# Optimization experiments

Hardware: AMD Instinct MI355X
Metric: run time of the kernel (lower is better)

The kernel has to match this reference:

```python
import jax, jax.numpy as jnp
import numpy as np

H = 1024
V = 5000
NUM_LAYERS = 2
B, T, U = 2, 128, 64


def setup_inputs() -> dict:
    key = jax.random.key(0)
    ks = jax.random.split(key, 16)
    s = 0.02
    inp = {
        "encoder_out": jax.random.normal(ks[0], (B, T, H), dtype=jnp.float32),
        "targets": jax.random.randint(ks[1], (B, U), 0, V),
        "embed": jax.random.normal(ks[2], (V, H), dtype=jnp.float32) * s,
        # stacked 2-layer LSTM params, PyTorch gate order (i, f, g, o)
        "lstm_Wih": jax.random.normal(ks[3], (NUM_LAYERS, 4 * H, H), dtype=jnp.float32) * s,
        "lstm_Whh": jax.random.normal(ks[4], (NUM_LAYERS, 4 * H, H), dtype=jnp.float32) * s,
        "lstm_bih": jnp.zeros((NUM_LAYERS, 4 * H), dtype=jnp.float32),
        "lstm_bhh": jnp.zeros((NUM_LAYERS, 4 * H), dtype=jnp.float32),
        "enc_W": jax.random.normal(ks[5], (H, H), dtype=jnp.float32) * s,
        "enc_b": jnp.zeros((H,), dtype=jnp.float32),
        "pred_W": jax.random.normal(ks[6], (H, H), dtype=jnp.float32) * s,
        "pred_b": jnp.zeros((H,), dtype=jnp.float32),
        "out_W": jax.random.normal(ks[7], (V + 1, H), dtype=jnp.float32) * s,
        "out_b": jnp.zeros((V + 1,), dtype=jnp.float32),
    }
    return inp


def _lstm_layer(x, Wih, Whh, bih, bhh):
    # x: [B, U, H] -> [B, U, H]; single LSTM layer, PyTorch gate order i,f,g,o
    b, u, h = x.shape
    bias = bih + bhh  # [4H]
    # precompute input projections for all timesteps: [U, B, 4H]
    xg = jnp.einsum('buh,gh->ubg', x, Wih) + bias

    def step(carry, xt):
        hprev, cprev = carry
        gates = xt + hprev @ Whh.T  # [B, 4H]
        i, f, g, o = jnp.split(gates, 4, axis=-1)
        i = jax.nn.sigmoid(i)
        f = jax.nn.sigmoid(f)
        g = jnp.tanh(g)
        o = jax.nn.sigmoid(o)
        c = f * cprev + i * g
        hnew = o * jnp.tanh(c)
        return (hnew, c), hnew

    init = (jnp.zeros((b, h), x.dtype), jnp.zeros((b, h), x.dtype))
    _, hs = jax.lax.scan(step, init, xg)  # hs: [U, B, H]
    return hs.transpose(1, 0, 2)


def reference(encoder_out, targets, embed, lstm_Wih, lstm_Whh, lstm_bih, lstm_bhh,
              enc_W, enc_b, pred_W, pred_b, out_W, out_b):
    # Prediction network: embedding + 2-layer LSTM (deterministic -> no dropout)
    x = embed[targets]  # [B, U, H]
    for l in range(NUM_LAYERS):
        x = _lstm_layer(x, lstm_Wih[l], lstm_Whh[l], lstm_bih[l], lstm_bhh[l])
    pred_out = x  # [B, U, H]

    # Joint network: proj + broadcast add over (T, U) + ReLU + output linear
    enc_p = jnp.einsum('bth,oh->bto', encoder_out, enc_W) + enc_b  # [B, T, H]
    prd_p = jnp.einsum('buh,oh->buo', pred_out, pred_W) + pred_b    # [B, U, H]
    joint = jax.nn.relu(enc_p[:, :, None, :] + prd_p[:, None, :, :])  # [B, T, U, H]
    logits = jnp.einsum('btuh,vh->btuv', joint, out_W) + out_b  # [B, T, U, V+1]
    return logits
```

## Files before the change

kernel.cpp:

```cpp
#include <hip/hip_runtime.h>
#include <hip/hip_bf16.h>

#define B_ 2
#define T_ 128
#define U_ 64
#define H_ 1024
#define NO_ 5001

typedef __attribute__((ext_vector_type(8))) short bf16x8;
typedef __attribute__((ext_vector_type(4))) float f32x4;

__device__ __forceinline__ float bf2f(unsigned short s) {
  unsigned int u = ((unsigned int)s) << 16;
  float f; __builtin_memcpy(&f, &u, 4); return f;
}
__device__ __forceinline__ unsigned short f2bf(float f) {
  unsigned int u; __builtin_memcpy(&u, &f, 4);
  u = u + 0x7FFFu + ((u >> 16) & 1u);
  return (unsigned short)(u >> 16);
}
__device__ __forceinline__ float fsig(float x) {
  x = fminf(fmaxf(x, -30.f), 30.f);
  float e = __expf(-x);
  return __builtin_amdgcn_rcpf(1.f + e);
}
__device__ __forceinline__ float ftanh(float x) {
  x = fminf(fmaxf(x, -15.f), 15.f);
  float e = __expf(2.f * x);
  return (e - 1.f) * __builtin_amdgcn_rcpf(e + 1.f);
}

__device__ __forceinline__ void gload_lds16(const unsigned short* g, unsigned short* l) {
  __builtin_amdgcn_global_load_lds(
      (const __attribute__((address_space(1))) unsigned int*)g,
      (__attribute__((address_space(3))) unsigned int*)l,
      16, 0, 0);
}

#define R_OUTW 1280256
#define R_WIH  (R_OUTW + 2097152)
#define R_WHH  (R_WIH + 2097152)
#define R_ENCW (R_WHH + 262144)
#define R_PRDW (R_ENCW + 262144)
#define R_ENC  (R_PRDW + 65536)
#define R_BIAS (R_ENC + 1280)

__global__ void k_cvt_all(
    const float* __restrict__ outW, const float* __restrict__ Wih,
    const float* __restrict__ Whh,  const float* __restrict__ encW,
    const float* __restrict__ prdW, const float* __restrict__ enc,
    const float* __restrict__ outB,
    unsigned short* __restrict__ outW_bf, unsigned short* __restrict__ Wih_bf,
    unsigned short* __restrict__ Whh_bf,  unsigned short* __restrict__ encW_bf,
    unsigned short* __restrict__ prdW_bf, unsigned short* __restrict__ enc_bf,
    float* __restrict__ biasPad)
{
  int i = blockIdx.x * 256 + threadIdx.x;
  const float* src; unsigned short* dst; int off;
  if (i < R_OUTW)      { src = outW; dst = outW_bf; off = i; }
  else if (i < R_WIH)  { src = Wih;  dst = Wih_bf;  off = i - R_OUTW; }
  else if (i < R_WHH)  { src = Whh;  dst = Whh_bf;  off = i - R_WIH; }
  else if (i < R_ENCW) { src = encW; dst = encW_bf; off = i - R_WHH; }
  else if (i < R_PRDW) { src = prdW; dst = prdW_bf; off = i - R_ENCW; }
  else if (i < R_ENC)  { src = enc;  dst = enc_bf;  off = i - R_PRDW; }
  else {
    int e0 = (i - R_ENC) * 4;
    float4 v;
    v.x = (e0 + 0 < NO_) ? outB[e0 + 0] : 0.f;
    v.y = (e0 + 1 < NO_) ? outB[e0 + 1] : 0.f;
    v.z = (e0 + 2 < NO_) ? outB[e0 + 2] : 0.f;
    v.w = (e0 + 3 < NO_) ? outB[e0 + 3] : 0.f;
    *(float4*)&biasPad[e0] = v;
    return;
  }
  const float4 v = ((const float4*)src)[off];
  ushort4 o;
  o.x = f2bf(v.x); o.y = f2bf(v.y); o.z = f2bf(v.z); o.w = f2bf(v.w);
  ((ushort4*)dst)[off] = o;
}

__global__ void k_embed(const int* __restrict__ tg, const float* __restrict__ em,
                        unsigned short* __restrict__ x0) {
  int idx = blockIdx.x * 256 + threadIdx.x;
  int bu = idx >> 8;
  int kc = (idx & 255) << 2;
  int t = tg[bu];
  const float4 v = *(const float4*)&em[(long)t * H_ + kc];
  ushort4 o; o.x = f2bf(v.x); o.y = f2bf(v.y); o.z = f2bf(v.z); o.w = f2bf(v.w);
  *(ushort4*)&x0[bu * H_ + kc] = o;
}

__global__ __launch_bounds__(256) void gemm_proj(
    const unsigned short* __restrict__ enc_bf, const unsigned short* __restrict__ x2_bf,
    const unsigned short* __restrict__ encW_bf, const unsigned short* __restrict__ prdW_bf,
    const float* __restrict__ encB, const float* __restrict__ prdB,
    float* __restrict__ ep, float* __restrict__ pp)
{
  __shared__ unsigned short As[128 * 32];
  __shared__ unsigned short Bs[128 * 32];
  const int tid = threadIdx.x;
  const unsigned short* A; const unsigned short* W; const float* b1; float* C;
  int m0;
  if (blockIdx.y < 2) { A = enc_bf; W = encW_bf; b1 = encB; C = ep; m0 = blockIdx.y * 128; }
  else                { A = x2_bf;  W = prdW_bf; b1 = prdB; C = pp; m0 = 0; }
  const int n0 = blockIdx.x * 128;
  const int K = H_, N = H_;
  const int lane = tid & 63, w = tid >> 6;
  const int wr = (w >> 1) * 64, wc = (w & 1) * 64;
  const int lr = lane & 15, lk = (lane >> 4) * 8;
  f32x4 acc[4][4] = {};

  for (int k0 = 0; k0 < K; k0 += 32) {
#pragma unroll
    for (int s = 0; s < 2; ++s) {
      int idx = (w * 2 + s) * 64 + lane;
      int row = idx >> 2, c8 = (idx & 3) * 8;
      gload_lds16(&A[(long)(m0 + row) * K + k0 + c8], &As[(w * 2 + s) * 512]);
      gload_lds16(&W[(long)(n0 + row) * K + k0 + c8], &Bs[(w * 2 + s) * 512]);
    }
    __syncthreads();
    bf16x8 aF[4], bF[4];
#pragma unroll
    for (int i = 0; i < 4; ++i) {
      aF[i] = *(const bf16x8*)&As[(wr + i * 16 + lr) * 32 + lk];
      bF[i] = *(const bf16x8*)&Bs[(wc + i * 16 + lr) * 32 + lk];
    }
#pragma unroll
    for (int i = 0; i < 4; ++i)
#pragma unroll
      for (int j = 0; j < 4; ++j)
        acc[i][j] = __builtin_amdgcn_mfma_f32_16x16x32_bf16(aF[i], bF[j], acc[i][j], 0, 0, 0);
    __syncthreads();
  }

  const int lq = (lane >> 4) * 4;
#pragma unroll
  for (int j = 0; j < 4; ++j) {
    int col = n0 + wc + j * 16 + lr;
    float bb = b1[col];
#pragma unroll
    for (int i = 0; i < 4; ++i) {
      int rowg = m0 + wr + i * 16 + lq;
#pragma unroll
      for (int r = 0; r < 4; ++r)
        C[(long)(rowg + r) * N + col] = acc[i][j][r] + bb;
    }
  }
}

#define STAGE_A(kt2, kh, rb) \
  gload_lds16(aSrc[rb] + (kt2) * 64 + (kh) * 32, \
              &As_f[((((kt2) & 1) * 2 + (kh)) * 8192) + ((rb) * 128 + wv * 16) * 32])
#define STAGE_B(kt2, kh, rb) \
  gload_lds16(bSrc[rb] + (kt2) * 64 + (kh) * 32, \
              &Bs_f[((((kt2) & 1) * 2 + (kh)) * 8192) + ((rb) * 128 + wv * 16) * 32])

__global__ __launch_bounds__(512, 1) void gemm_logits(
    const unsigned short* __restrict__ A, const unsigned short* __restrict__ W,
    const float* __restrict__ biasPad, float* __restrict__ C, int M, int N, int K)
{
  __shared__ __align__(16) unsigned short lds_all[65536];
  unsigned short* As_f = lds_all;
  unsigned short* Bs_f = lds_all + 32768;
  const int tid = threadIdx.x;
  const int lane = tid & 63, wv = tid >> 6;
  const int wm = wv >> 2, wn = wv & 3;
  int swzb = (blockIdx.x & 7) * 160 + (blockIdx.x >> 3);
  const int n0 = (swzb >> 6) * 256;
  const int m0 = (swzb & 63) * 256;
  const int NT = K / 64;

  const unsigned short* aSrc[2];
  const unsigned short* bSrc[2];
#pragma unroll
  for (int rb = 0; rb < 2; ++rb) {
    int rl = rb * 128 + (tid >> 2);
    int c2s = (tid & 3) ^ ((rl >> 1) & 3);
    aSrc[rb] = A + (long)(m0 + rl) * K + c2s * 8;
    bSrc[rb] = W + (long)(n0 + rl) * K + c2s * 8;
  }
  int aOff[8], bOff[4];
#pragma unroll
  for (int i = 0; i < 8; ++i) {
    int r = wm * 128 + i * 16 + (lane & 15);
    aOff[i] = r * 32 + (((lane >> 4) ^ ((r >> 1) & 3)) * 8);
  }
#pragma unroll
  for (int j = 0; j < 4; ++j) {
    int r = wn * 64 + j * 16 + (lane & 15);
    bOff[j] = r * 32 + (((lane >> 4) ^ ((r >> 1) & 3)) * 8);
  }

  f32x4 acc[8][4] = {};

  STAGE_A(0, 0, 0); STAGE_A(0, 0, 1); STAGE_B(0, 0, 0); STAGE_B(0, 0, 1);
  STAGE_A(0, 1, 0); STAGE_A(0, 1, 1); STAGE_B(0, 1, 0); STAGE_B(0, 1, 1);

  for (int kt = 0; kt < NT; ++kt) {
    const int b = kt & 1;
    asm volatile("s_waitcnt vmcnt(4)" ::: "memory");
    __builtin_amdgcn_s_barrier();
    __builtin_amdgcn_sched_barrier(0);
    {
      const int base = (b * 2 + 0) * 8192;
      bf16x8 aF[8], bF[4];
#pragma unroll
      for (int i = 0; i < 8; ++i) aF[i] = *(const bf16x8*)&As_f[base + aOff[i]];
#pragma unroll
      for (int j = 0; j < 4; ++j) bF[j] = *(const bf16x8*)&Bs_f[base + bOff[j]];
      if (kt + 1 < NT) {
        STAGE_A(kt + 1, 0, 0); STAGE_A(kt + 1, 0, 1);
        STAGE_B(kt + 1, 0, 0); STAGE_B(kt + 1, 0, 1);
        STAGE_A(kt + 1, 1, 0); STAGE_A(kt + 1, 1, 1);
      }
      __builtin_amdgcn_s_setprio(1);
#pragma unroll
      for (int i = 0; i < 8; ++i)
#pragma unroll
        for (int j = 0; j < 4; ++j)
          acc[i][j] = __builtin_amdgcn_mfma_f32_16x16x32_bf16(aF[i], bF[j], acc[i][j], 0, 0, 0);
      __builtin_amdgcn_s_setprio(0);
    }
    if (kt + 1 < NT) { asm volatile("s_waitcnt vmcnt(6)" ::: "memory"); }
    else             { asm volatile("s_waitcnt vmcnt(0)" ::: "memory"); }
    __builtin_amdgcn_s_barrier();
    __builtin_amdgcn_sched_barrier(0);
    {
      const int base = (b * 2 + 1) * 8192;
      bf16x8 aF[8], bF[4];
#pragma unroll
      for (int i = 0; i < 8; ++i) aF[i] = *(const bf16x8*)&As_f[base + aOff[i]];
#pragma unroll
      for (int j = 0; j < 4; ++j) bF[j] = *(const bf16x8*)&Bs_f[base + bOff[j]];
      if (kt + 1 < NT) { STAGE_B(kt + 1, 1, 0); STAGE_B(kt + 1, 1, 1); }
      __builtin_amdgcn_s_setprio(1);
#pragma unroll
      for (int i = 0; i < 8; ++i)
#pragma unroll
        for (int j = 0; j < 4; ++j)
          acc[i][j] = __builtin_amdgcn_mfma_f32_16x16x32_bf16(aF[i], bF[j], acc[i][j], 0, 0, 0);
      __builtin_amdgcn_s_setprio(0);
    }
  }

  float* eb = (float*)lds_all;
  const int lq = (lane >> 4) * 4;
  float bv4[4];
#pragma unroll
  for (int j = 0; j < 4; ++j) bv4[j] = biasPad[n0 + wn * 64 + j * 16 + (lane & 15)];

#pragma unroll
  for (int cp = 0; cp < 4; ++cp) {
    __syncthreads();
#pragma unroll
    for (int ii = 0; ii < 2; ++ii) {
      int rbase = wm * 32 + ii * 16 + lq;
#pragma unroll
      for (int j = 0; j < 4; ++j) {
        int col = wn * 64 + j * 16 + (lane & 15);
#pragma unroll
        for (int r = 0; r < 4; ++r)
          eb[(rbase + r) * 261 + col] = acc[cp * 2 + ii][j][r] + bv4[j];
      }
    }
    __syncthreads();
    {
      int rl = tid >> 3, ci = tid & 7;
      long grow = (long)m0 + (rl >> 5) * 128 + cp * 32 + (rl & 31);
      float* crow = C + grow * N + n0;
      const float* er = &eb[rl * 261];
#pragma unroll
      for (int k = 0; k < 8; ++k) {
        int col = ci * 4 + k * 32;
        float4 v = *(const float4*)&er[col];
        int gc = n0 + col;
        if (gc + 4 <= N) {
          *(float4*)&crow[col] = v;
        } else if (gc < N) {
          float tmp[4] = {v.x, v.y, v.z, v.w};
#pragma unroll
          for (int e = 0; e < 4; ++e)
            if (gc + e < N) crow[col + e] = tmp[e];
        }
      }
    }
  }
}

__global__ __launch_bounds__(256, 1) void lstm_fused3(
    const unsigned short* __restrict__ x0_bf,
    const unsigned short* __restrict__ Whh0,
    const unsigned short* __restrict__ Wih0,
    const unsigned short* __restrict__ Whh1,
    const unsigned short* __restrict__ Wih1,
    const float* __restrict__ bih0, const float* __restrict__ bhh0,
    const float* __restrict__ bih1, const float* __restrict__ bhh1,
    unsigned short* __restrict__ x2_bf,
    float* __restrict__ hbuf0,
    float* __restrict__ hbuf1,
    float* __restrict__ xbuf,
    float* __restrict__ xg1buf, int* __restrict__ flags1,
    float* __restrict__ xg0buf, int* __restrict__ flags0)
{
  __shared__ float hs[2][H_];
  __shared__ float part[2][4][64][2];
  __shared__ float biasS[64];

  const int tid = threadIdx.x;
  const int grp = blockIdx.x >> 6;
  const int bid = blockIdx.x & 63;
  const int w = tid >> 6, l = tid & 63;
  const int g = l >> 4, q = l & 15;
  const int row = g * 1024 + bid * 16 + q;
  const int kb = w * 256;

#define DOT_BODY(WREG, SRC)                                                              \
  _Pragma("unroll")                                                                      \
  for (int it = 0; it < 32; ++it) {                                                      \
    bf16x8 wv = WREG[it];                                                                \
    float4 h0a = *(const float4*)&SRC[0][kb + it * 8];                                   \
    float4 h0b = *(const float4*)&SRC[0][kb + it * 8 + 4];                               \
    float4 h1a = *(const float4*)&SRC[1][kb + it * 8];                                   \
    float4 h1b = *(const float4*)&SRC[1][kb + it * 8 + 4];                               \
    a00 += bf2f((unsigned short)wv[0]) * h0a.x + bf2f((unsigned short)wv[4]) * h0b.x;    \
    a01 += bf2f((unsigned short)wv[1]) * h0a.y + bf2f((unsigned short)wv[5]) * h0b.y;    \
    a02 += bf2f((unsigned short)wv[2]) * h0a.z + bf2f((unsigned short)wv[6]) * h0b.z;    \
    a03 += bf2f((unsigned short)wv[3]) * h0a.w + bf2f((unsigned short)wv[7]) * h0b.w;    \
    a10 += bf2f((unsigned short)wv[0]) * h1a.x + bf2f((unsigned short)wv[4]) * h1b.x;    \
    a11 += bf2f((unsigned short)wv[1]) * h1a.y + bf2f((unsigned short)wv[5]) * h1b.y;    \
    a12 += bf2f((unsigned short)wv[2]) * h1a.z + bf2f((unsigned short)wv[6]) * h1b.z;    \
    a13 += bf2f((unsigned short)wv[3]) * h1a.w + bf2f((unsigned short)wv[7]) * h1b.w;    \
  }

  if (grp == 0 || grp == 2) {
    const unsigned short* Whh = (grp == 0) ? Whh0 : Whh1;
    float* hbuf   = (grp == 0) ? hbuf0 : hbuf1;
    const float* xgbufR = (grp == 0) ? xg0buf : xg1buf;
    const int* flagsR   = (grp == 0) ? flags0 : flags1;
    bf16x8 wreg[32];
#pragma unroll
    for (int it = 0; it < 32; ++it)
      wreg[it] = *(const bf16x8*)&Whh[(long)row * H_ + kb + it * 8];
    __syncthreads();

    float creg = 0.f;
    for (int u = 0; u < U_; ++u) {
      const int p = u & 1;
      float xgi = 0.f, xgf = 0.f, xgg = 0.f, xgo = 0.f;
      if (tid < 32) {
        const int* fp = &flagsR[(u * 64 + bid) * 16];
        int fv;
        for (;;) {
          asm volatile("global_load_dword %0, %1, off sc1\n\ts_waitcnt vmcnt(0)"
                       : "=v"(fv) : "v"(fp) : "memory");
          if (fv != 0) break;
          __builtin_amdgcn_s_sleep(8);
        }
        const float* xb = &xgbufR[((u * 64 + bid) * 2 + (tid >> 4)) * 64];
        int qq = tid & 15;
        asm volatile("global_load_dword %0, %1, off sc1" : "=&v"(xgi) : "v"(xb + qq) : "memory");
        asm volatile("global_load_dword %0, %1, off sc1" : "=&v"(xgf) : "v"(xb + 16 + qq) : "memory");
        asm volatile("global_load_dword %0, %1, off sc1" : "=&v"(xgg) : "v"(xb + 32 + qq) : "memory");
        asm volatile("global_load_dword %0, %1, off sc1" : "=&v"(xgo) : "v"(xb + 48 + qq) : "memory");
      }
      float a00 = 0.f, a01 = 0.f, a02 = 0.f, a03 = 0.f;
      float a10 = 0.f, a11 = 0.f, a12 = 0.f, a13 = 0.f;
      if (u > 0) {
        const float thr = 4.0f * u - 2.0f;
        const float* base = hbuf + (u & 1) * 2 * H_;
        const float* pa = base + tid * 4;
        const float* pb = base + H_ + tid * 4;
        float4 va, vb;
        for (;;) {
          asm volatile("global_load_dwordx4 %0, %2, off sc1\n\t"
                       "global_load_dwordx4 %1, %3, off sc1\n\t"
                       "s_waitcnt vmcnt(0)"
                       : "=v"(va), "=v"(vb) : "v"(pa), "v"(pb) : "memory");
          if (va.x > thr && va.y > thr && va.z > thr && va.w > thr &&
              vb.x > thr && vb.y > thr && vb.z > thr && vb.w > thr) break;
          __builtin_amdgcn_s_sleep(8);
        }
        const float off = 4.0f * u;
        va.x -= off; va.y -= off; va.z -= off; va.w -= off;
        vb.x -= off; vb.y -= off; vb.z -= off; vb.w -= off;
        *(float4*)&hs[0][tid * 4] = va;
        *(float4*)&hs[1][tid * 4] = vb;
        DOT_BODY(wreg, hs)
      }
      part[p][w][l][0] = (a00 + a01) + (a02 + a03);
      part[p][w][l][1] = (a10 + a11) + (a12 + a13);
      if (tid < 32) {
        asm volatile("s_waitcnt vmcnt(0)"
                     : "+v"(xgi), "+v"(xgf), "+v"(xgg), "+v"(xgo) :: "memory");
      }
      __syncthreads();
      if (tid < 32) {
        int b = tid >> 4, qq = tid & 15;
        float gi = part[p][0][qq][b] + part[p][1][qq][b] + part[p][2][qq][b]
                 + part[p][3][qq][b] + xgi;
        float gf = part[p][0][16 + qq][b] + part[p][1][16 + qq][b] + part[p][2][16 + qq][b]
                 + part[p][3][16 + qq][b] + xgf;
        float gc = part[p][0][32 + qq][b] + part[p][1][32 + qq][b] + part[p][2][32 + qq][b]
                 + part[p][3][32 + qq][b] + xgg;
        float go = part[p][0][48 + qq][b] + part[p][1][48 + qq][b] + part[p][2][48 + qq][b]
                 + part[p][3][48 + qq][b] + xgo;
        float i_ = fsig(gi), f_ = fsig(gf), g_ = ftanh(gc), o_ = fsig(go);
        creg = f_ * creg + i_ * g_;
        float h = o_ * ftanh(creg);
        int j = bid * 16 + qq;
        if (grp == 0) {
          float tvx = h + 4.0f;
          const float* px = &xbuf[u * 2 * H_ + b * H_ + j];
          asm volatile("global_store_dword %0, %1, off sc1" :: "v"(px), "v"(tvx) : "memory");
        } else {
          x2_bf[(b * U_ + u) * H_ + j] = f2bf(h);
        }
        if (u < U_ - 1) {
          float tv = h + 4.0f * (u + 1);
          const float* pp2 = &hbuf[((u + 1) & 1) * 2 * H_ + b * H_ + j];
          asm volatile("global_store_dword %0, %1, off sc1" :: "v"(pp2), "v"(tv) : "memory");
        }
      }
    }
  } else {
    const bool isX1 = (grp == 1);
    const unsigned short* Wih = isX1 ? Wih1 : Wih0;
    const float* bihp = isX1 ? bih1 : bih0;
    const float* bhhp = isX1 ? bhh1 : bhh0;
    float* xgbufW = isX1 ? xg1buf : xg0buf;
    int* flagsW   = isX1 ? flags1 : flags0;
    bf16x8 wreg[32];
#pragma unroll
    for (int it = 0; it < 32; ++it)
      wreg[it] = *(const bf16x8*)&Wih[(long)row * H_ + kb + it * 8];
    if (tid < 64) {
      int rr = (tid >> 4) * 1024 + bid * 16 + (tid & 15);
      biasS[tid] = bihp[rr] + bhhp[rr];
    }
    __syncthreads();

    for (int u = 0; u < U_; ++u) {
      const int p = u & 1;
      if (isX1) {
        const float* base = xbuf + u * 2 * H_;
        const float* pa = base + tid * 4;
        const float* pb = base + H_ + tid * 4;
        float4 va, vb;
        for (;;) {
          asm volatile("global_load_dwordx4 %0, %2, off sc1\n\t"
                       "global_load_dwordx4 %1, %3, off sc1\n\t"
                       "s_waitcnt vmcnt(0)"
                       : "=v"(va), "=v"(vb) : "v"(pa), "v"(pb) : "memory");
          if (va.x > 2.f && va.y > 2.f && va.z > 2.f && va.w > 2.f &&
              vb.x > 2.f && vb.y > 2.f && vb.z > 2.f && vb.w > 2.f) break;
          __builtin_amdgcn_s_sleep(8);
        }
        va.x -= 4.f; va.y -= 4.f; va.z -= 4.f; va.w -= 4.f;
        vb.x -= 4.f; vb.y -= 4.f; vb.z -= 4.f; vb.w -= 4.f;
        *(float4*)&hs[0][tid * 4] = va;
        *(float4*)&hs[1][tid * 4] = vb;
      } else {
        ushort4 xa = *(const ushort4*)&x0_bf[(0 * U_ + u) * H_ + tid * 4];
        ushort4 xb = *(const ushort4*)&x0_bf[(1 * U_ + u) * H_ + tid * 4];
        float4 va, vb;
        va.x = bf2f(xa.x); va.y = bf2f(xa.y); va.z = bf2f(xa.z); va.w = bf2f(xa.w);
        vb.x = bf2f(xb.x); vb.y = bf2f(xb.y); vb.z = bf2f(xb.z); vb.w = bf2f(xb.w);
        *(float4*)&hs[0][tid * 4] = va;
        *(float4*)&hs[1][tid * 4] = vb;
      }

      float a00 = 0.f, a01 = 0.f, a02 = 0.f, a03 = 0.f;
      float a10 = 0.f, a11 = 0.f, a12 = 0.f, a13 = 0.f;
      DOT_BODY(wreg, hs)
      part[p][w][l][0] = (a00 + a01) + (a02 + a03);
      part[p][w][l][1] = (a10 + a11) + (a12 + a13);
      __syncthreads();
      if (tid < 128) {
        int b = tid >> 6, ll = tid & 63;
        float s = part[p][0][ll][b] + part[p][1][ll][b] + part[p][2][ll][b]
                + part[p][3][ll][b] + biasS[ll];
        const float* pw = &xgbufW[((u * 64 + bid) * 2 + b) * 64 + ll];
        asm volatile("global_store_dword %0, %1, off sc1" :: "v"(pw), "v"(s) : "memory");
        asm volatile("s_waitcnt vmcnt(0)" ::: "memory");
      }
      __syncthreads();
      if (tid == 0) {
        int one = 1;
        const int* fp = &flagsW[(u * 64 + bid) * 16];
        asm volatile("global_store_dword %0, %1, off sc1" :: "v"(fp), "v"(one) : "memory");
      }
    }
  }
#undef DOT_BODY
}

__global__ void k_joint(const float* __restrict__ ep, const float* __restrict__ pp,
                        unsigned short* __restrict__ jt)
{
  int idx = blockIdx.x * 256 + threadIdx.x;
  int m = idx >> 8;
  int kc = (idx & 255) << 2;
  int erow = m >> 6;
  int prow = (m >> 13) * U_ + (m & 63);
  const float4 e = *(const float4*)&ep[erow * H_ + kc];
  const float4 p = *(const float4*)&pp[prow * H_ + kc];
  float4 s;
  s.x = fmaxf(e.x + p.x, 0.f); s.y = fmaxf(e.y + p.y, 0.f);
  s.z = fmaxf(e.z + p.z, 0.f); s.w = fmaxf(e.w + p.w, 0.f);
  ushort4 o; o.x = f2bf(s.x); o.y = f2bf(s.y); o.z = f2bf(s.z); o.w = f2bf(s.w);
  *(ushort4*)&jt[m * H_ + kc] = o;
}

extern "C" void kernel_launch(void* const* d_in, const int* in_sizes, int n_in,
                              void* d_out, int out_size, void* d_ws, size_t ws_size,
                              hipStream_t stream)
{
  const float* enc   = (const float*)d_in[0];
  const int*   tg    = (const int*)d_in[1];
  const float* em    = (const float*)d_in[2];
  const float* Wih   = (const float*)d_in[3];
  const float* Whh   = (const float*)d_in[4];
  const float* bih   = (const float*)d_in[5];
  const float* bhh   = (const float*)d_in[6];
  const float* encW  = (const float*)d_in[7];
  const float* encB  = (const float*)d_in[8];
  const float* prdW  = (const float*)d_in[9];
  const float* prdB  = (const float*)d_in[10];
  const float* outW  = (const float*)d_in[11];
  const float* outB  = (const float*)d_in[12];
  float* out = (float*)d_out;
  char* ws = (char*)d_ws;

  unsigned short* outW_bf = (unsigned short*)(ws + 0);
  unsigned short* Wih_bf  = (unsigned short*)(ws + 10485760);
  unsigned short* Whh_bf  = (unsigned short*)(ws + 27262976);
  unsigned short* encW_bf = (unsigned short*)(ws + 44040192);
  unsigned short* prdW_bf = (unsigned short*)(ws + 46137344);
  unsigned short* enc_bf  = (unsigned short*)(ws + 48234496);
  unsigned short* x0_bf   = (unsigned short*)(ws + 48758784);
  unsigned short* x2_bf   = (unsigned short*)(ws + 49283072);
  float* xg1buf = (float*)(ws + 49545216);
  float* hbufL0 = (float*)(ws + 51642368);
  unsigned short* jt = (unsigned short*)(ws + 51659008);
  int*   flags0 = (int*)(ws + 51659008);
  float* xg0buf = (float*)(ws + 51659008 + 262144);
  float* hbufL1 = (float*)(ws + 85213440);
  float* biasPad = (float*)(ws + 85229824);
  float* xbuf = (float*)(ws + 85250304);
  int* flags1 = (int*)(ws + 85774592);
  float* ep = (float*)(ws + 49545216);
  float* pp = (float*)(ws + 49545216 + 1048576);

  hipMemsetAsync(hbufL0, 0, 16384, stream);
  hipMemsetAsync(hbufL1, 0, 86036736 - 85213440, stream);
  hipMemsetAsync(flags0, 0, 262144, stream);

  k_cvt_all<<<R_BIAS / 256, 256, 0, stream>>>(
      outW, Wih, Whh, encW, prdW, enc, outB,
      outW_bf, Wih_bf, Whh_bf, encW_bf, prdW_bf, enc_bf, biasPad);
  k_embed<<<(B_ * U_ * H_ / 4) / 256, 256, 0, stream>>>(tg, em, x0_bf);

  lstm_fused3<<<256, 256, 0, stream>>>(
      x0_bf,
      Whh_bf, Wih_bf,
      Whh_bf + 4096 * H_, Wih_bf + 4096 * H_,
      bih, bhh, bih + 4096, bhh + 4096,
      x2_bf, hbufL0, hbufL1, xbuf,
      xg1buf, flags1, xg0buf, flags0);

  gemm_proj<<<dim3(8, 3), 256, 0, stream>>>(enc_bf, x2_bf, encW_bf, prdW_bf,
                                            encB, prdB, ep, pp);

  k_joint<<<16384, 256, 0, stream>>>(ep, pp, jt);
  gemm_logits<<<1280, 512, 0, stream>>>(jt, outW_bf, biasPad, out, B_ * T_ * U_, NO_, H_);
}
```

Before: 599.5 us.

## Fuse pred projection and joint logits GEMM into persistent LSTM megakernel

Merges the LSTM, the prediction projection and the logits GEMM into one persistent kernel. Extra blocks consume per-timestep LSTM outputs through flag and tag polling, so the projection and the output GEMM overlap with the sequential recurrence. The joint add+ReLU is done on the fly while staging the A tile, which removes the materialised joint buffer. The cost is replacing the tuned 256x256 double-buffered logits GEMM with a simple 128x128 single-buffer loop. Correctness and progress also depend on all 592 blocks being co-resident so the spin-waits cannot deadlock.

```diff
diff --git a/kernel.cpp b/kernel.cpp
--- a/kernel.cpp
+++ b/kernel.cpp
@@ -90,20 +90,14 @@
   *(ushort4*)&x0[bu * H_ + kc] = o;
 }
 
-__global__ __launch_bounds__(256) void gemm_proj(
-    const unsigned short* __restrict__ enc_bf, const unsigned short* __restrict__ x2_bf,
-    const unsigned short* __restrict__ encW_bf, const unsigned short* __restrict__ prdW_bf,
-    const float* __restrict__ encB, const float* __restrict__ prdB,
-    float* __restrict__ ep, float* __restrict__ pp)
+__global__ __launch_bounds__(256) void gemm_ep(
+    const unsigned short* __restrict__ enc_bf, const unsigned short* __restrict__ encW_bf,
+    const float* __restrict__ encB, float* __restrict__ ep)
 {
   __shared__ unsigned short As[128 * 32];
   __shared__ unsigned short Bs[128 * 32];
   const int tid = threadIdx.x;
-  const unsigned short* A; const unsigned short* W; const float* b1; float* C;
-  int m0;
-  if (blockIdx.y < 2) { A = enc_bf; W = encW_bf; b1 = encB; C = ep; m0 = blockIdx.y * 128; }
-  else                { A = x2_bf;  W = prdW_bf; b1 = prdB; C = pp; m0 = 0; }
-  const int n0 = blockIdx.x * 128;
+  const int n0 = blockIdx.x * 128, m0 = blockIdx.y * 128;
   const int K = H_, N = H_;
   const int lane = tid & 63, w = tid >> 6;
   const int wr = (w >> 1) * 64, wc = (w & 1) * 64;
@@ -115,8 +109,8 @@
     for (int s = 0; s < 2; ++s) {
       int idx = (w * 2 + s) * 64 + lane;
       int row = idx >> 2, c8 = (idx & 3) * 8;
-      gload_lds16(&A[(long)(m0 + row) * K + k0 + c8], &As[(w * 2 + s) * 512]);
-      gload_lds16(&W[(long)(n0 + row) * K + k0 + c8], &Bs[(w * 2 + s) * 512]);
+      gload_lds16(&enc_bf[(long)(m0 + row) * K + k0 + c8], &As[(w * 2 + s) * 512]);
+      gload_lds16(&encW_bf[(long)(n0 + row) * K + k0 + c8], &Bs[(w * 2 + s) * 512]);
     }
     __syncthreads();
     bf16x8 aF[4], bF[4];
@@ -137,177 +131,40 @@
 #pragma unroll
   for (int j = 0; j < 4; ++j) {
     int col = n0 + wc + j * 16 + lr;
-    float bb = b1[col];
+    float bb = encB[col];
 #pragma unroll
     for (int i = 0; i < 4; ++i) {
       int rowg = m0 + wr + i * 16 + lq;
 #pragma unroll
       for (int r = 0; r < 4; ++r)
-        C[(long)(rowg + r) * N + col] = acc[i][j][r] + bb;
+        ep[(long)(rowg + r) * N + col] = acc[i][j][r] + bb;
     }
   }
 }
 
-#define STAGE_A(kt2, kh, rb) \
-  gload_lds16(aSrc[rb] + (kt2) * 64 + (kh) * 32, \
-              &As_f[((((kt2) & 1) * 2 + (kh)) * 8192) + ((rb) * 128 + wv * 16) * 32])
-#define STAGE_B(kt2, kh, rb) \
-  gload_lds16(bSrc[rb] + (kt2) * 64 + (kh) * 32, \
-              &Bs_f[((((kt2) & 1) * 2 + (kh)) * 8192) + ((rb) * 128 + wv * 16) * 32])
-
-__global__ __launch_bounds__(512, 1) void gemm_logits(
-    const unsigned short* __restrict__ A, const unsigned short* __restrict__ W,
-    const float* __restrict__ biasPad, float* __restrict__ C, int M, int N, int K)
-{
-  __shared__ __align__(16) unsigned short lds_all[65536];
-  unsigned short* As_f = lds_all;
-  unsigned short* Bs_f = lds_all + 32768;
-  const int tid = threadIdx.x;
-  const int lane = tid & 63, wv = tid >> 6;
-  const int wm = wv >> 2, wn = wv & 3;
-  int swzb = (blockIdx.x & 7) * 160 + (blockIdx.x >> 3);
-  const int n0 = (swzb >> 6) * 256;
-  const int m0 = (swzb & 63) * 256;
-  const int NT = K / 64;
-
-  const unsigned short* aSrc[2];
-  const unsigned short* bSrc[2];
-#pragma unroll
-  for (int rb = 0; rb < 2; ++rb) {
-    int rl = rb * 128 + (tid >> 2);
-    int c2s = (tid & 3) ^ ((rl >> 1) & 3);
-    aSrc[rb] = A + (long)(m0 + rl) * K + c2s * 8;
-    bSrc[rb] = W + (long)(n0 + rl) * K + c2s * 8;
-  }
-  int aOff[8], bOff[4];
-#pragma unroll
-  for (int i = 0; i < 8; ++i) {
-    int r = wm * 128 + i * 16 + (lane & 15);
-    aOff[i] = r * 32 + (((lane >> 4) ^ ((r >> 1) & 3)) * 8);
-  }
-#pragma unroll
-  for (int j = 0; j < 4; ++j) {
-    int r = wn * 64 + j * 16 + (lane & 15);
-    bOff[j] = r * 32 + (((lane >> 4) ^ ((r >> 1) & 3)) * 8);
-  }
-
-  f32x4 acc[8][4] = {};
-
-  STAGE_A(0, 0, 0); STAGE_A(0, 0, 1); STAGE_B(0, 0, 0); STAGE_B(0, 0, 1);
-  STAGE_A(0, 1, 0); STAGE_A(0, 1, 1); STAGE_B(0, 1, 0); STAGE_B(0, 1, 1);
-
-  for (int kt = 0; kt < NT; ++kt) {
-    const int b = kt & 1;
-    asm volatile("s_waitcnt vmcnt(4)" ::: "memory");
-    __builtin_amdgcn_s_barrier();
-    __builtin_amdgcn_sched_barrier(0);
-    {
-      const int base = (b * 2 + 0) * 8192;
-      bf16x8 aF[8], bF[4];
-#pragma unroll
-      for (int i = 0; i < 8; ++i) aF[i] = *(const bf16x8*)&As_f[base + aOff[i]];
-#pragma unroll
-      for (int j = 0; j < 4; ++j) bF[j] = *(const bf16x8*)&Bs_f[base + bOff[j]];
-      if (kt + 1 < NT) {
-        STAGE_A(kt + 1, 0, 0); STAGE_A(kt + 1, 0, 1);
-        STAGE_B(kt + 1, 0, 0); STAGE_B(kt + 1, 0, 1);
-        STAGE_A(kt + 1, 1, 0); STAGE_A(kt + 1, 1, 1);
-      }
-      __builtin_amdgcn_s_setprio(1);
-#pragma unroll
-      for (int i = 0; i < 8; ++i)
-#pragma unroll
-        for (int j = 0; j < 4; ++j)
-          acc[i][j] = __builtin_amdgcn_mfma_f32_16x16x32_bf16(aF[i], bF[j], acc[i][j], 0, 0, 0);
-      __builtin_amdgcn_s_setprio(0);
-    }
-    if (kt + 1 < NT) { asm volatile("s_waitcnt vmcnt(6)" ::: "memory"); }
-    else             { asm volatile("s_waitcnt vmcnt(0)" ::: "memory"); }
-    __builtin_amdgcn_s_barrier();
-    __builtin_amdgcn_sched_barrier(0);
-    {
-      const int base = (b * 2 + 1) * 8192;
-      bf16x8 aF[8], bF[4];
-#pragma unroll
-      for (int i = 0; i < 8; ++i) aF[i] = *(const bf16x8*)&As_f[base + aOff[i]];
-#pragma unroll
-      for (int j = 0; j < 4; ++j) bF[j] = *(const bf16x8*)&Bs_f[base + bOff[j]];
-      if (kt + 1 < NT) { STAGE_B(kt + 1, 1, 0); STAGE_B(kt + 1, 1, 1); }
-      __builtin_amdgcn_s_setprio(1);
-#pragma unroll
-      for (int i = 0; i < 8; ++i)
-#pragma unroll
-        for (int j = 0; j < 4; ++j)
-          acc[i][j] = __builtin_amdgcn_mfma_f32_16x16x32_bf16(aF[i], bF[j], acc[i][j], 0, 0, 0);
-      __builtin_amdgcn_s_setprio(0);
-    }
-  }
-
-  float* eb = (float*)lds_all;
-  const int lq = (lane >> 4) * 4;
-  float bv4[4];
-#pragma unroll
-  for (int j = 0; j < 4; ++j) bv4[j] = biasPad[n0 + wn * 64 + j * 16 + (lane & 15)];
-
-#pragma unroll
-  for (int cp = 0; cp < 4; ++cp) {
-    __syncthreads();
-#pragma unroll
-    for (int ii = 0; ii < 2; ++ii) {
-      int rbase = wm * 32 + ii * 16 + lq;
-#pragma unroll
-      for (int j = 0; j < 4; ++j) {
-        int col = wn * 64 + j * 16 + (lane & 15);
-#pragma unroll
-        for (int r = 0; r < 4; ++r)
-          eb[(rbase + r) * 261 + col] = acc[cp * 2 + ii][j][r] + bv4[j];
-      }
-    }
-    __syncthreads();
-    {
-      int rl = tid >> 3, ci = tid & 7;
-      long grow = (long)m0 + (rl >> 5) * 128 + cp * 32 + (rl & 31);
-      float* crow = C + grow * N + n0;
-      const float* er = &eb[rl * 261];
-#pragma unroll
-      for (int k = 0; k < 8; ++k) {
-        int col = ci * 4 + k * 32;
-        float4 v = *(const float4*)&er[col];
-        int gc = n0 + col;
-        if (gc + 4 <= N) {
-          *(float4*)&crow[col] = v;
-        } else if (gc < N) {
-          float tmp[4] = {v.x, v.y, v.z, v.w};
-#pragma unroll
-          for (int e = 0; e < 4; ++e)
-            if (gc + e < N) crow[col + e] = tmp[e];
-        }
-      }
-    }
-  }
-}
-
-__global__ __launch_bounds__(256, 1) void lstm_fused3(
+__global__ __launch_bounds__(256, 1) void mega(
     const unsigned short* __restrict__ x0_bf,
-    const unsigned short* __restrict__ Whh0,
-    const unsigned short* __restrict__ Wih0,
-    const unsigned short* __restrict__ Whh1,
-    const unsigned short* __restrict__ Wih1,
+    const unsigned short* __restrict__ Whh0, const unsigned short* __restrict__ Wih0,
+    const unsigned short* __restrict__ Whh1, const unsigned short* __restrict__ Wih1,
+    const unsigned short* __restrict__ prdW_bf, const unsigned short* __restrict__ outW_bf,
     const float* __restrict__ bih0, const float* __restrict__ bhh0,
     const float* __restrict__ bih1, const float* __restrict__ bhh1,
-    unsigned short* __restrict__ x2_bf,
-    float* __restrict__ hbuf0,
-    float* __restrict__ hbuf1,
+    const float* __restrict__ prdB, const float* __restrict__ biasPad,
+    const float* __restrict__ ep,
+    float* __restrict__ hbuf0, float* __restrict__ hbuf1,
     float* __restrict__ xbuf,
     float* __restrict__ xg1buf, int* __restrict__ flags1,
-    float* __restrict__ xg0buf, int* __restrict__ flags0)
+    float* __restrict__ xg0buf, int* __restrict__ flags0,
+    float* __restrict__ x2tag,
+    float* __restrict__ ppbuf, int* __restrict__ flagsP,
+    float* __restrict__ out)
 {
-  __shared__ float hs[2][H_];
-  __shared__ float part[2][4][64][2];
-  __shared__ float biasS[64];
+  __shared__ __align__(16) char smem[20992];
+  float (*hs)[H_] = (float(*)[H_])smem;
+  float (*part)[4][64][2] = (float(*)[4][64][2])(smem + 8192);
+  float* biasS = (float*)(smem + 8192 + 4096);
 
   const int tid = threadIdx.x;
-  const int grp = blockIdx.x >> 6;
   const int bid = blockIdx.x & 63;
   const int w = tid >> 6, l = tid & 63;
   const int g = l >> 4, q = l & 15;
@@ -332,7 +189,8 @@
     a13 += bf2f((unsigned short)wv[3]) * h1a.w + bf2f((unsigned short)wv[7]) * h1b.w;    \
   }
 
-  if (grp == 0 || grp == 2) {
+  if (blockIdx.x < 256 && ((blockIdx.x >> 6) == 0 || (blockIdx.x >> 6) == 2)) {
+    const int grp = blockIdx.x >> 6;
     const unsigned short* Whh = (grp == 0) ? Whh0 : Whh1;
     float* hbuf   = (grp == 0) ? hbuf0 : hbuf1;
     const float* xgbufR = (grp == 0) ? xg0buf : xg1buf;
@@ -408,12 +266,13 @@
         creg = f_ * creg + i_ * g_;
         float h = o_ * ftanh(creg);
         int j = bid * 16 + qq;
+        float tvx = h + 4.0f;
         if (grp == 0) {
-          float tvx = h + 4.0f;
           const float* px = &xbuf[u * 2 * H_ + b * H_ + j];
           asm volatile("global_store_dword %0, %1, off sc1" :: "v"(px), "v"(tvx) : "memory");
         } else {
-          x2_bf[(b * U_ + u) * H_ + j] = f2bf(h);
+          const float* px = &x2tag[u * 2 * H_ + b * H_ + j];
+          asm volatile("global_store_dword %0, %1, off sc1" :: "v"(px), "v"(tvx) : "memory");
         }
         if (u < U_ - 1) {
           float tv = h + 4.0f * (u + 1);
@@ -422,8 +281,8 @@
         }
       }
     }
-  } else {
-    const bool isX1 = (grp == 1);
+  } else if (blockIdx.x < 256) {
+    const bool isX1 = ((blockIdx.x >> 6) == 1);
     const unsigned short* Wih = isX1 ? Wih1 : Wih0;
     const float* bihp = isX1 ? bih1 : bih0;
     const float* bhhp = isX1 ? bhh1 : bhh0;
@@ -490,25 +349,179 @@
         asm volatile("global_store_dword %0, %1, off sc1" :: "v"(fp), "v"(one) : "memory");
       }
     }
+  } else if (blockIdx.x < 272) {
+    const int pbid = blockIdx.x - 256;
+    bf16x8 wreg[32];
+#pragma unroll
+    for (int it = 0; it < 32; ++it)
+      wreg[it] = *(const bf16x8*)&prdW_bf[(long)(pbid * 64 + l) * H_ + kb + it * 8];
+    if (tid < 64) biasS[tid] = prdB[pbid * 64 + tid];
+    __syncthreads();
+
+    for (int u = 0; u < U_; ++u) {
+      const int p = u & 1;
+      const float* base = x2tag + u * 2 * H_;
+      const float* pa = base + tid * 4;
+      const float* pb = base + H_ + tid * 4;
+      float4 va, vb;
+      for (;;) {
+        asm volatile("global_load_dwordx4 %0, %2, off sc1\n\t"
+                     "global_load_dwordx4 %1, %3, off sc1\n\t"
+                     "s_waitcnt vmcnt(0)"
+                     : "=v"(va), "=v"(vb) : "v"(pa), "v"(pb) : "memory");
+        if (va.x > 2.f && va.y > 2.f && va.z > 2.f && va.w > 2.f &&
+            vb.x > 2.f && vb.y > 2.f && vb.z > 2.f && vb.w > 2.f) break;
+        __builtin_amdgcn_s_sleep(8);
+      }
+      va.x -= 4.f; va.y -= 4.f; va.z -= 4.f; va.w -= 4.f;
+      vb.x -= 4.f; vb.y -= 4.f; vb.z -= 4.f; vb.w -= 4.f;
+      *(float4*)&hs[0][tid * 4] = va;
+      *(float4*)&hs[1][tid * 4] = vb;
+
+      float a00 = 0.f, a01 = 0.f, a02 = 0.f, a03 = 0.f;
+      float a10 = 0.f, a11 = 0.f, a12 = 0.f, a13 = 0.f;
+      DOT_BODY(wreg, hs)
+      part[p][w][l][0] = (a00 + a01) + (a02 + a03);
+      part[p][w][l][1] = (a10 + a11) + (a12 + a13);
+      __syncthreads();
+      if (tid < 128) {
+        int b = tid >> 6, ll = tid & 63;
+        float s = part[p][0][ll][b] + part[p][1][ll][b] + part[p][2][ll][b]
+                + part[p][3][ll][b] + biasS[ll];
+        const float* pw = &ppbuf[((u * 16 + pbid) * 2 + b) * 64 + ll];
+        asm volatile("global_store_dword %0, %1, off sc1" :: "v"(pw), "v"(s) : "memory");
+        asm volatile("s_waitcnt vmcnt(0)" ::: "memory");
+      }
+      __syncthreads();
+      if (tid == 0) {
+        int one = 1;
+        const int* fp = &flagsP[(u * 16 + pbid) * 16];
+        asm volatile("global_store_dword %0, %1, off sc1" :: "v"(fp), "v"(one) : "memory");
+      }
+    }
+  } else {
+    const int lgid = blockIdx.x - 272;
+    const int col80 = lgid % 80;
+    const int uc = lgid / 80;
+    const int bb = col80 & 1;
+    const int np = col80 >> 1;
+    const int n0 = np * 128;
+    unsigned short* As = (unsigned short*)smem;
+    unsigned short* Bs = (unsigned short*)(smem + 8192);
+    float* eb  = (float*)smem;
+    float* pps = (float*)(smem + 16896);
+    const int lane = tid & 63, w4 = tid >> 6;
+    const int wr = (w4 >> 1) * 64, wc = (w4 & 1) * 64;
+    const int lr = lane & 15, lk = (lane >> 4) * 8;
+    const int lq = (lane >> 4) * 4;
+    float bv[4];
+#pragma unroll
+    for (int j = 0; j < 4; ++j) bv[j] = biasPad[n0 + wc + j * 16 + lr];
+
+    for (int u = uc * 16; u < uc * 16 + 16; ++u) {
+      {
+        int fv = 1;
+        const int* fp = &flagsP[(u * 16 + (lane & 15)) * 16];
+        for (;;) {
+          if (lane < 16) {
+            asm volatile("global_load_dword %0, %1, off sc1\n\ts_waitcnt vmcnt(0)"
+                         : "=v"(fv) : "v"(fp) : "memory");
+          }
+          if (__all(fv != 0)) break;
+          __builtin_amdgcn_s_sleep(8);
+        }
+      }
+      __syncthreads();
+      {
+        int col = tid * 4, pbid = col >> 6, off = col & 63;
+        const float* pa2 = &ppbuf[((u * 16 + pbid) * 2 + bb) * 64 + off];
+        float4 pv;
+        asm volatile("global_load_dwordx4 %0, %1, off sc1\n\ts_waitcnt vmcnt(0)"
+                     : "=v"(pv) : "v"(pa2) : "memory");
+        *(float4*)&pps[col] = pv;
+      }
+      __syncthreads();
+
+      f32x4 acc[4][4] = {};
+      for (int kt = 0; kt < 32; ++kt) {
+        const int k0 = kt * 32;
+#pragma unroll
+        for (int rep = 0; rep < 4; ++rep) {
+          int idx = rep * 256 + tid;
+          int arow = idx >> 3, c4 = (idx & 7) * 4;
+          float4 ev = *(const float4*)&ep[(long)(bb * 128 + arow) * H_ + k0 + c4];
+          float4 pv = *(const float4*)&pps[k0 + c4];
+          ushort4 o;
+          o.x = f2bf(fmaxf(ev.x + pv.x, 0.f));
+          o.y = f2bf(fmaxf(ev.y + pv.y, 0.f));
+          o.z = f2bf(fmaxf(ev.z + pv.z, 0.f));
+          o.w = f2bf(fmaxf(ev.w + pv.w, 0.f));
+          *(ushort4*)&As[arow * 32 + c4] = o;
+        }
+#pragma unroll
+        for (int s2 = 0; s2 < 2; ++s2) {
+          int idx = (w4 * 2 + s2) * 64 + lane;
+          int brow = idx >> 2, c8 = (idx & 3) * 8;
+          gload_lds16(&outW_bf[(long)(n0 + brow) * H_ + k0 + c8], &Bs[(w4 * 2 + s2) * 512]);
+        }
+        __syncthreads();
+        bf16x8 aF[4], bF[4];
+#pragma unroll
+        for (int i = 0; i < 4; ++i) {
+          aF[i] = *(const bf16x8*)&As[(wr + i * 16 + lr) * 32 + lk];
+          bF[i] = *(const bf16x8*)&Bs[(wc + i * 16 + lr) * 32 + lk];
+        }
+#pragma unroll
+        for (int i = 0; i < 4; ++i)
+#pragma unroll
+          for (int j = 0; j < 4; ++j)
+            acc[i][j] = __builtin_amdgcn_mfma_f32_16x16x32_bf16(aF[i], bF[j], acc[i][j], 0, 0, 0);
+        __syncthreads();
+      }
+#pragma unroll
+      for (int cp = 0; cp < 4; ++cp) {
+        __syncthreads();
+        if ((wr == 0) == (cp < 2)) {
+#pragma unroll
+          for (int ii = 0; ii < 2; ++ii) {
+            int i = (cp & 1) * 2 + ii;
+#pragma unroll
+            for (int j = 0; j < 4; ++j) {
+              int col = wc + j * 16 + lr;
+#pragma unroll
+              for (int r = 0; r < 4; ++r) {
+                int lrow = wr + i * 16 + lq + r - cp * 32;
+                eb[lrow * 132 + col] = acc[i][j][r] + bv[j];
+              }
+            }
+          }
+        }
+        __syncthreads();
+        {
+          int rt = tid >> 3, ci = tid & 7;
+          int trow = cp * 32 + rt;
+          long grow = ((long)(bb * 128 + trow)) * 64 + u;
+          float* crow = out + grow * NO_ + n0;
+          const float* er = &eb[rt * 132];
+#pragma unroll
+          for (int k2 = 0; k2 < 4; ++k2) {
+            int col = ci * 4 + k2 * 32;
+            float4 v = *(const float4*)&er[col];
+            int gc = n0 + col;
+            if (gc + 4 <= NO_) {
+              *(float4*)&crow[col] = v;
+            } else if (gc < NO_) {
+              float tmp[4] = {v.x, v.y, v.z, v.w};
+#pragma unroll
+              for (int e = 0; e < 4; ++e)
+                if (gc + e < NO_) crow[col + e] = tmp[e];
+            }
+          }
+        }
+      }
+    }
   }
 #undef DOT_BODY
-}
-
-__global__ void k_joint(const float* __restrict__ ep, const float* __restrict__ pp,
-                        unsigned short* __restrict__ jt)
-{
-  int idx = blockIdx.x * 256 + threadIdx.x;
-  int m = idx >> 8;
-  int kc = (idx & 255) << 2;
-  int erow = m >> 6;
-  int prow = (m >> 13) * U_ + (m & 63);
-  const float4 e = *(const float4*)&ep[erow * H_ + kc];
-  const float4 p = *(const float4*)&pp[prow * H_ + kc];
-  float4 s;
-  s.x = fmaxf(e.x + p.x, 0.f); s.y = fmaxf(e.y + p.y, 0.f);
-  s.z = fmaxf(e.z + p.z, 0.f); s.w = fmaxf(e.w + p.w, 0.f);
-  ushort4 o; o.x = f2bf(s.x); o.y = f2bf(s.y); o.z = f2bf(s.z); o.w = f2bf(s.w);
-  *(ushort4*)&jt[m * H_ + kc] = o;
 }
 
 extern "C" void kernel_launch(void* const* d_in, const int* in_sizes, int n_in,
@@ -538,39 +551,39 @@
   unsigned short* prdW_bf = (unsigned short*)(ws + 46137344);
   unsigned short* enc_bf  = (unsigned short*)(ws + 48234496);
   unsigned short* x0_bf   = (unsigned short*)(ws + 48758784);
-  unsigned short* x2_bf   = (unsigned short*)(ws + 49283072);
   float* xg1buf = (float*)(ws + 49545216);
   float* hbufL0 = (float*)(ws + 51642368);
-  unsigned short* jt = (unsigned short*)(ws + 51659008);
   int*   flags0 = (int*)(ws + 51659008);
-  float* xg0buf = (float*)(ws + 51659008 + 262144);
+  float* xg0buf = (float*)(ws + 51921152);
+  float* x2tag  = (float*)(ws + 54018304);
+  float* ppbuf  = (float*)(ws + 54542592);
+  int*   flagsP = (int*)(ws + 55066880);
+  float* ep     = (float*)(ws + 55132416);
   float* hbufL1 = (float*)(ws + 85213440);
   float* biasPad = (float*)(ws + 85229824);
   float* xbuf = (float*)(ws + 85250304);
   int* flags1 = (int*)(ws + 85774592);
-  float* ep = (float*)(ws + 49545216);
-  float* pp = (float*)(ws + 49545216 + 1048576);
 
   hipMemsetAsync(hbufL0, 0, 16384, stream);
   hipMemsetAsync(hbufL1, 0, 86036736 - 85213440, stream);
   hipMemsetAsync(flags0, 0, 262144, stream);
+  hipMemsetAsync(x2tag, 0, 524288, stream);
+  hipMemsetAsync(flagsP, 0, 65536, stream);
 
   k_cvt_all<<<R_BIAS / 256, 256, 0, stream>>>(
       outW, Wih, Whh, encW, prdW, enc, outB,
       outW_bf, Wih_bf, Whh_bf, encW_bf, prdW_bf, enc_bf, biasPad);
   k_embed<<<(B_ * U_ * H_ / 4) / 256, 256, 0, stream>>>(tg, em, x0_bf);
-
-  lstm_fused3<<<256, 256, 0, stream>>>(
+  gemm_ep<<<dim3(8, 2), 256, 0, stream>>>(enc_bf, encW_bf, encB, ep);
+
+  mega<<<592, 256, 0, stream>>>(
       x0_bf,
       Whh_bf, Wih_bf,
       Whh_bf + 4096 * H_, Wih_bf + 4096 * H_,
+      prdW_bf, outW_bf,
       bih, bhh, bih + 4096, bhh + 4096,
-      x2_bf, hbufL0, hbufL1, xbuf,
-      xg1buf, flags1, xg0buf, flags0);
-
-  gemm_proj<<<dim3(8, 3), 256, 0, stream>>>(enc_bf, x2_bf, encW_bf, prdW_bf,
-                                            encB, prdB, ep, pp);
-
-  k_joint<<<16384, 256, 0, stream>>>(ep, pp, jt);
-  gemm_logits<<<1280, 512, 0, stream>>>(jt, outW_bf, biasPad, out, B_ * T_ * U_, NO_, H_);
-}
+      prdB, biasPad, ep,
+      hbufL0, hbufL1, xbuf,
+      xg1buf, flags1, xg0buf, flags0,
+      x2tag, ppbuf, flagsP, out);
+}
```

Measured after the change: 1.519 ms. 2.53x slower.

## Fuse joint add+ReLU into logits GEMM A-tile build; merge embed into convert kernel

Applied to the files above, without the earlier changes.

The separate joint kernel, which wrote a 16384x1024 bf16 tensor, is removed. The logits GEMM now builds its A tiles directly from the fp32 encoder and prediction projections, doing the add, ReLU and bf16 conversion while storing into LDS. This avoids writing and re-reading a 32MB intermediate, at the cost of synchronous register loads and ALU work inside the pipelined GEMM loop in place of async global-to-LDS loads. The embedding gather is also folded into the conversion kernel to save one launch.

```diff
diff --git a/kernel.cpp b/kernel.cpp
--- a/kernel.cpp
+++ b/kernel.cpp
@@ -44,16 +44,18 @@
 #define R_PRDW (R_ENCW + 262144)
 #define R_ENC  (R_PRDW + 65536)
 #define R_BIAS (R_ENC + 1280)
+#define R_EMB  (R_BIAS + 32768)
 
 __global__ void k_cvt_all(
     const float* __restrict__ outW, const float* __restrict__ Wih,
     const float* __restrict__ Whh,  const float* __restrict__ encW,
     const float* __restrict__ prdW, const float* __restrict__ enc,
     const float* __restrict__ outB,
+    const int* __restrict__ tg, const float* __restrict__ em,
     unsigned short* __restrict__ outW_bf, unsigned short* __restrict__ Wih_bf,
     unsigned short* __restrict__ Whh_bf,  unsigned short* __restrict__ encW_bf,
     unsigned short* __restrict__ prdW_bf, unsigned short* __restrict__ enc_bf,
-    float* __restrict__ biasPad)
+    float* __restrict__ biasPad, unsigned short* __restrict__ x0_bf)
 {
   int i = blockIdx.x * 256 + threadIdx.x;
   const float* src; unsigned short* dst; int off;
@@ -63,7 +65,7 @@
   else if (i < R_ENCW) { src = encW; dst = encW_bf; off = i - R_WHH; }
   else if (i < R_PRDW) { src = prdW; dst = prdW_bf; off = i - R_ENCW; }
   else if (i < R_ENC)  { src = enc;  dst = enc_bf;  off = i - R_PRDW; }
-  else {
+  else if (i < R_BIAS) {
     int e0 = (i - R_ENC) * 4;
     float4 v;
     v.x = (e0 + 0 < NO_) ? outB[e0 + 0] : 0.f;
@@ -72,22 +74,20 @@
     v.w = (e0 + 3 < NO_) ? outB[e0 + 3] : 0.f;
     *(float4*)&biasPad[e0] = v;
     return;
+  } else {
+    int idx = i - R_BIAS;
+    int bu = idx >> 8;
+    int kc = (idx & 255) << 2;
+    int t = tg[bu];
+    const float4 v = *(const float4*)&em[(long)t * H_ + kc];
+    ushort4 o; o.x = f2bf(v.x); o.y = f2bf(v.y); o.z = f2bf(v.z); o.w = f2bf(v.w);
+    *(ushort4*)&x0_bf[bu * H_ + kc] = o;
+    return;
   }
   const float4 v = ((const float4*)src)[off];
   ushort4 o;
   o.x = f2bf(v.x); o.y = f2bf(v.y); o.z = f2bf(v.z); o.w = f2bf(v.w);
   ((ushort4*)dst)[off] = o;
-}
-
-__global__ void k_embed(const int* __restrict__ tg, const float* __restrict__ em,
-                        unsigned short* __restrict__ x0) {
-  int idx = blockIdx.x * 256 + threadIdx.x;
-  int bu = idx >> 8;
-  int kc = (idx & 255) << 2;
-  int t = tg[bu];
-  const float4 v = *(const float4*)&em[(long)t * H_ + kc];
-  ushort4 o; o.x = f2bf(v.x); o.y = f2bf(v.y); o.z = f2bf(v.z); o.w = f2bf(v.w);
-  *(ushort4*)&x0[bu * H_ + kc] = o;
 }
 
 __global__ __launch_bounds__(256) void gemm_proj(
@@ -148,16 +148,14 @@
   }
 }
 
-#define STAGE_A(kt2, kh, rb) \
-  gload_lds16(aSrc[rb] + (kt2) * 64 + (kh) * 32, \
-              &As_f[((((kt2) & 1) * 2 + (kh)) * 8192) + ((rb) * 128 + wv * 16) * 32])
 #define STAGE_B(kt2, kh, rb) \
   gload_lds16(bSrc[rb] + (kt2) * 64 + (kh) * 32, \
               &Bs_f[((((kt2) & 1) * 2 + (kh)) * 8192) + ((rb) * 128 + wv * 16) * 32])
 
-__global__ __launch_bounds__(512, 1) void gemm_logits(
-    const unsigned short* __restrict__ A, const unsigned short* __restrict__ W,
-    const float* __restrict__ biasPad, float* __restrict__ C, int M, int N, int K)
+__global__ __launch_bounds__(512, 1) void gemm_logits_f(
+    const float* __restrict__ ep, const float* __restrict__ pp,
+    const unsigned short* __restrict__ W,
+    const float* __restrict__ biasPad, float* __restrict__ C)
 {
   __shared__ __align__(16) unsigned short lds_all[65536];
   unsigned short* As_f = lds_all;
@@ -168,16 +166,15 @@
   int swzb = (blockIdx.x & 7) * 160 + (blockIdx.x >> 3);
   const int n0 = (swzb >> 6) * 256;
   const int m0 = (swzb & 63) * 256;
-  const int NT = K / 64;
-
-  const unsigned short* aSrc[2];
+  const int NT = H_ / 64;
+  const int N = NO_;
+
   const unsigned short* bSrc[2];
 #pragma unroll
   for (int rb = 0; rb < 2; ++rb) {
     int rl = rb * 128 + (tid >> 2);
     int c2s = (tid & 3) ^ ((rl >> 1) & 3);
-    aSrc[rb] = A + (long)(m0 + rl) * K + c2s * 8;
-    bSrc[rb] = W + (long)(n0 + rl) * K + c2s * 8;
+    bSrc[rb] = W + (long)(n0 + rl) * H_ + c2s * 8;
   }
   int aOff[8], bOff[4];
 #pragma unroll
@@ -191,14 +188,47 @@
     bOff[j] = r * 32 + (((lane >> 4) ^ ((r >> 1) & 3)) * 8);
   }
 
+  const int rA = tid >> 1;
+  const int halfa = tid & 1;
+  const float* eprow = ep + (long)((m0 >> 6) + (rA >> 6)) * H_;
+  const float* pprow = pp + (long)(((m0 >> 13) << 6) + (rA & 63)) * H_;
+  const int abase = rA * 32;
+  const int axor = (rA >> 1) & 3;
+
+  auto BUILD_A = [&](int kt2, int kh) {
+    const int k0 = kt2 * 64 + kh * 32;
+    const int bufb = ((kt2 & 1) * 2 + kh) * 8192;
+#pragma unroll
+    for (int s = 0; s < 2; ++s) {
+      int cc = halfa * 2 + s;
+      int c8 = k0 + cc * 8;
+      float4 e0 = *(const float4*)&eprow[c8];
+      float4 e1 = *(const float4*)&eprow[c8 + 4];
+      float4 p0 = *(const float4*)&pprow[c8];
+      float4 p1 = *(const float4*)&pprow[c8 + 4];
+      ushort4 o0, o1;
+      o0.x = f2bf(fmaxf(e0.x + p0.x, 0.f));
+      o0.y = f2bf(fmaxf(e0.y + p0.y, 0.f));
+      o0.z = f2bf(fmaxf(e0.z + p0.z, 0.f));
+      o0.w = f2bf(fmaxf(e0.w + p0.w, 0.f));
+      o1.x = f2bf(fmaxf(e1.x + p1.x, 0.f));
+      o1.y = f2bf(fmaxf(e1.y + p1.y, 0.f));
+      o1.z = f2bf(fmaxf(e1.z + p1.z, 0.f));
+      o1.w = f2bf(fmaxf(e1.w + p1.w, 0.f));
+      int slot = cc ^ axor;
+      *(ushort4*)&As_f[bufb + abase + slot * 8] = o0;
+      *(ushort4*)&As_f[bufb + abase + slot * 8 + 4] = o1;
+    }
+  };
+
   f32x4 acc[8][4] = {};
 
-  STAGE_A(0, 0, 0); STAGE_A(0, 0, 1); STAGE_B(0, 0, 0); STAGE_B(0, 0, 1);
-  STAGE_A(0, 1, 0); STAGE_A(0, 1, 1); STAGE_B(0, 1, 0); STAGE_B(0, 1, 1);
+  BUILD_A(0, 0); BUILD_A(0, 1);
+  STAGE_B(0, 0, 0); STAGE_B(0, 0, 1); STAGE_B(0, 1, 0); STAGE_B(0, 1, 1);
 
   for (int kt = 0; kt < NT; ++kt) {
     const int b = kt & 1;
-    asm volatile("s_waitcnt vmcnt(4)" ::: "memory");
+    asm volatile("s_waitcnt vmcnt(2)" ::: "memory");
     __builtin_amdgcn_s_barrier();
     __builtin_amdgcn_sched_barrier(0);
     {
@@ -209,9 +239,8 @@
 #pragma unroll
       for (int j = 0; j < 4; ++j) bF[j] = *(const bf16x8*)&Bs_f[base + bOff[j]];
       if (kt + 1 < NT) {
-        STAGE_A(kt + 1, 0, 0); STAGE_A(kt + 1, 0, 1);
+        BUILD_A(kt + 1, 0);
         STAGE_B(kt + 1, 0, 0); STAGE_B(kt + 1, 0, 1);
-        STAGE_A(kt + 1, 1, 0); STAGE_A(kt + 1, 1, 1);
       }
       __builtin_amdgcn_s_setprio(1);
 #pragma unroll
@@ -221,7 +250,7 @@
           acc[i][j] = __builtin_amdgcn_mfma_f32_16x16x32_bf16(aF[i], bF[j], acc[i][j], 0, 0, 0);
       __builtin_amdgcn_s_setprio(0);
     }
-    if (kt + 1 < NT) { asm volatile("s_waitcnt vmcnt(6)" ::: "memory"); }
+    if (kt + 1 < NT) { asm volatile("s_waitcnt vmcnt(2)" ::: "memory"); }
     else             { asm volatile("s_waitcnt vmcnt(0)" ::: "memory"); }
     __builtin_amdgcn_s_barrier();
     __builtin_amdgcn_sched_barrier(0);
@@ -232,7 +261,10 @@
       for (int i = 0; i < 8; ++i) aF[i] = *(const bf16x8*)&As_f[base + aOff[i]];
 #pragma unroll
       for (int j = 0; j < 4; ++j) bF[j] = *(const bf16x8*)&Bs_f[base + bOff[j]];
-      if (kt + 1 < NT) { STAGE_B(kt + 1, 1, 0); STAGE_B(kt + 1, 1, 1); }
+      if (kt + 1 < NT) {
+        BUILD_A(kt + 1, 1);
+        STAGE_B(kt + 1, 1, 0); STAGE_B(kt + 1, 1, 1);
+      }
       __builtin_amdgcn_s_setprio(1);
 #pragma unroll
       for (int i = 0; i < 8; ++i)
@@ -494,23 +526,6 @@
 #undef DOT_BODY
 }
 
-__global__ void k_joint(const float* __restrict__ ep, const float* __restrict__ pp,
-                        unsigned short* __restrict__ jt)
-{
-  int idx = blockIdx.x * 256 + threadIdx.x;
-  int m = idx >> 8;
-  int kc = (idx & 255) << 2;
-  int erow = m >> 6;
-  int prow = (m >> 13) * U_ + (m & 63);
-  const float4 e = *(const float4*)&ep[erow * H_ + kc];
-  const float4 p = *(const float4*)&pp[prow * H_ + kc];
-  float4 s;
-  s.x = fmaxf(e.x + p.x, 0.f); s.y = fmaxf(e.y + p.y, 0.f);
-  s.z = fmaxf(e.z + p.z, 0.f); s.w = fmaxf(e.w + p.w, 0.f);
-  ushort4 o; o.x = f2bf(s.x); o.y = f2bf(s.y); o.z = f2bf(s.z); o.w = f2bf(s.w);
-  *(ushort4*)&jt[m * H_ + kc] = o;
-}
-
 extern "C" void kernel_launch(void* const* d_in, const int* in_sizes, int n_in,
                               void* d_out, int out_size, void* d_ws, size_t ws_size,
                               hipStream_t stream)
@@ -541,9 +556,8 @@
   unsigned short* x2_bf   = (unsigned short*)(ws + 49283072);
   float* xg1buf = (float*)(ws + 49545216);
   float* hbufL0 = (float*)(ws + 51642368);
-  unsigned short* jt = (unsigned short*)(ws + 51659008);
   int*   flags0 = (int*)(ws + 51659008);
-  float* xg0buf = (float*)(ws + 51659008 + 262144);
+  float* xg0buf = (float*)(ws + 51921152);
   float* hbufL1 = (float*)(ws + 85213440);
   float* biasPad = (float*)(ws + 85229824);
   float* xbuf = (float*)(ws + 85250304);
@@ -555,10 +569,9 @@
   hipMemsetAsync(hbufL1, 0, 86036736 - 85213440, stream);
   hipMemsetAsync(flags0, 0, 262144, stream);
 
-  k_cvt_all<<<R_BIAS / 256, 256, 0, stream>>>(
-      outW, Wih, Whh, encW, prdW, enc, outB,
-      outW_bf, Wih_bf, Whh_bf, encW_bf, prdW_bf, enc_bf, biasPad);
-  k_embed<<<(B_ * U_ * H_ / 4) / 256, 256, 0, stream>>>(tg, em, x0_bf);
+  k_cvt_all<<<R_EMB / 256, 256, 0, stream>>>(
+      outW, Wih, Whh, encW, prdW, enc, outB, tg, em,
+      outW_bf, Wih_bf, Whh_bf, encW_bf, prdW_bf, enc_bf, biasPad, x0_bf);
 
   lstm_fused3<<<256, 256, 0, stream>>>(
       x0_bf,
@@ -571,6 +584,5 @@
   gemm_proj<<<dim3(8, 3), 256, 0, stream>>>(enc_bf, x2_bf, encW_bf, prdW_bf,
                                             encB, prdB, ep, pp);
 
-  k_joint<<<16384, 256, 0, stream>>>(ep, pp, jt);
-  gemm_logits<<<1280, 512, 0, stream>>>(jt, outW_bf, biasPad, out, B_ * T_ * U_, NO_, H_);
-}
+  gemm_logits_f<<<1280, 512, 0, stream>>>(ep, pp, outW_bf, biasPad, out);
+}
```

After: 682.2 us. 1.14x slower.
